# Kernel tuning notes

Measured on AMD Instinct MI355X. Metric: run time of the kernel, lower is better.

## Reference

```python
import jax, jax.numpy as jnp
import numpy as np

B, T, E, H = 8, 2048, 1024, 128

def setup_inputs() -> dict:
    key = jax.random.key(0)
    k1, k2, k3, k4 = jax.random.split(key, 4)
    s = 0.02
    return {
        "x":  jax.random.normal(k1, (B, T, E), dtype=jnp.float32),
        "Wq": jax.random.normal(k2, (E, H), dtype=jnp.float32) * s,
        "Wk": jax.random.normal(k3, (E, H), dtype=jnp.float32) * s,
        "Wv": jax.random.normal(k4, (E, H), dtype=jnp.float32) * s,
    }

def reference(x, Wq, Wk, Wv):
    # q,k,v: [B,T,H]
    q = jnp.einsum("bte,eh->bth", x, Wq)
    k = jnp.einsum("bte,eh->bth", x, Wk)
    v = jnp.einsum("bte,eh->bth", x, Wv)
    scale = jnp.asarray(q.shape[-1], q.dtype) ** -0.5
    wei = jnp.einsum("bqh,bkh->bqk", q, k) * scale  # [B,T,T]
    causal = jnp.tril(jnp.ones((wei.shape[1], wei.shape[2]), dtype=bool))
    wei = jnp.where(causal, wei, jnp.asarray(-jnp.inf, wei.dtype))
    wei = jax.nn.softmax(wei, axis=-1)
    # dropout_prob = 0.0 -> identity
    return jnp.einsum("bqk,bkh->bqh", wei, v)
```

## Files before the change

kernel.cpp:

```cpp
#include <hip/hip_runtime.h>

#define BB 8
#define TT 2048
#define EE 1024
#define HH 128

typedef __bf16 bf16;
typedef __attribute__((ext_vector_type(8))) __bf16 bf16x8;
typedef __attribute__((ext_vector_type(4))) __bf16 bf16x4;
typedef __attribute__((ext_vector_type(4))) float f32x4;
typedef __attribute__((ext_vector_type(16))) float f32x16;

__device__ __host__ inline int qb_off(int qb) {
  int h = qb >> 1;
  return qb + h * (h - 1) + ((qb & 1) ? h : 0);
}
#define NSLAB 72

__device__ inline void gload_lds16(const bf16* g, bf16* l) {
  __builtin_amdgcn_global_load_lds((const __attribute__((address_space(1))) unsigned int*)g,
                                   (__attribute__((address_space(3))) unsigned int*)l,
                                   16, 0, 0);
}

__global__ __launch_bounds__(256) void wt_kernel(const float* __restrict__ wq,
                                                 const float* __restrict__ wk,
                                                 const float* __restrict__ wv,
                                                 bf16* __restrict__ wt) {
  __shared__ float tile[64][65];
  const int z = blockIdx.z;
  const float* w = (z == 0) ? wq : ((z == 1) ? wk : wv);
  const int k0 = blockIdx.x * 64;
  const int h0 = blockIdx.y * 64;
  const int c = threadIdx.x & 63;
  const int r0 = threadIdx.x >> 6;
#pragma unroll
  for (int i = 0; i < 16; ++i) {
    int tt = r0 + i * 4;
    tile[tt][c] = w[(size_t)(k0 + tt) * HH + h0 + c];
  }
  __syncthreads();
#pragma unroll
  for (int i = 0; i < 16; ++i) {
    int hh = r0 + i * 4;
    wt[((size_t)(z * HH + h0 + hh)) * EE + k0 + c] = (bf16)tile[c][hh];
  }
}

__global__ __launch_bounds__(256) void xcvt_kernel(const float* __restrict__ x,
                                                   bf16* __restrict__ xb) {
  const size_t base = (size_t)blockIdx.x * 4096 + threadIdx.x * 4;
#pragma unroll
  for (int j = 0; j < 4; ++j) {
    size_t idx = base + j * 1024;
    f32x4 xv = *(const f32x4*)(x + idx);
    bf16x4 xo;
#pragma unroll
    for (int i = 0; i < 4; ++i) xo[i] = (bf16)xv[i];
    *(bf16x4*)(xb + idx) = xo;
  }
}

__global__ __launch_bounds__(256) void gemm_kernel(const bf16* __restrict__ xb,
                                                   const bf16* __restrict__ wt,
                                                   bf16* __restrict__ q,
                                                   bf16* __restrict__ k,
                                                   bf16* __restrict__ v) {
  __shared__ bf16 As[128 * 32];
  __shared__ bf16 Bs[96 * 32];
  const int tid = threadIdx.x;
  const int lane = tid & 63;
  const int wave = tid >> 6;
  const int l16 = lane & 15;
  const int quad = lane >> 4;
  const int wm = wave & 1;
  const int wn = wave >> 1;
  const int bm = blockIdx.x;
  const int ntile = blockIdx.y;

  const int trow = tid >> 2;
  const int tsub = (tid & 3) * 8;
  const bf16* gA = xb + (size_t)(bm * 128 + trow) * EE + tsub;
  const bf16* gB = wt + (size_t)(ntile * 96 + trow) * EE + tsub;

  f32x4 acc[4][3];
#pragma unroll
  for (int rg = 0; rg < 4; ++rg)
#pragma unroll
    for (int nt = 0; nt < 3; ++nt) acc[rg][nt] = f32x4{0.f, 0.f, 0.f, 0.f};

  for (int ks = 0; ks < EE / 32; ++ks) {
    gload_lds16(gA + ks * 32, &As[wave * 512]);
    gload_lds16(gA + (size_t)64 * EE + ks * 32, &As[2048 + wave * 512]);
    gload_lds16(gB + ks * 32, &Bs[wave * 512]);
    if (tid < 128)
      gload_lds16(gB + (size_t)64 * EE + ks * 32, &Bs[2048 + wave * 512]);
    __syncthreads();

    bf16x8 af[4], bf[3];
#pragma unroll
    for (int rg = 0; rg < 4; ++rg)
      af[rg] = *(const bf16x8*)&As[(wm * 64 + rg * 16 + l16) * 32 + quad * 8];
#pragma unroll
    for (int nt = 0; nt < 3; ++nt)
      bf[nt] = *(const bf16x8*)&Bs[(wn * 48 + nt * 16 + l16) * 32 + quad * 8];
#pragma unroll
    for (int rg = 0; rg < 4; ++rg)
#pragma unroll
      for (int nt = 0; nt < 3; ++nt)
        acc[rg][nt] = __builtin_amdgcn_mfma_f32_16x16x32_bf16(af[rg], bf[nt], acc[rg][nt], 0, 0, 0);
    __syncthreads();
  }

  bf16* outp[3] = {q, k, v};
#pragma unroll
  for (int rg = 0; rg < 4; ++rg)
#pragma unroll
    for (int nt = 0; nt < 3; ++nt) {
      int col = ntile * 96 + wn * 48 + nt * 16 + l16;
      int z = col >> 7;
      int n = col & 127;
#pragma unroll
      for (int r = 0; r < 4; ++r) {
        int row = bm * 128 + wm * 64 + rg * 16 + quad * 4 + r;
        outp[z][(size_t)row * HH + n] = (bf16)acc[rg][nt][r];
      }
    }
}

__global__ __launch_bounds__(256) void vtrans_kernel(const bf16* __restrict__ v,
                                                     bf16* __restrict__ vt) {
  __shared__ bf16 tile[64][65];
  const int b = blockIdx.x;
  const int t0 = blockIdx.y * 64;
  const int h0 = blockIdx.z * 64;
  const int c = threadIdx.x & 63;
  const int r0 = threadIdx.x >> 6;
#pragma unroll
  for (int i = 0; i < 16; ++i) {
    int tt = r0 + i * 4;
    tile[tt][c] = v[((size_t)(b * TT + t0 + tt)) * HH + h0 + c];
  }
  __syncthreads();
#pragma unroll
  for (int i = 0; i < 16; ++i) {
    int hh = r0 + i * 4;
    vt[((size_t)(b * HH + h0 + hh)) * TT + t0 + c] = tile[c][hh];
  }
}


__device__ __forceinline__ unsigned pk2(float a, float b) {
  union { __bf16 h[2]; unsigned u; } x;
  x.h[0] = (__bf16)a;
  x.h[1] = (__bf16)b;
  return x.u;
}

__device__ __forceinline__ void plswap(unsigned& a, unsigned& b) {
  asm volatile("v_permlane32_swap_b32 %0, %1" : "+v"(a), "+v"(b));
}

__global__ __launch_bounds__(256, 2) void flash_kernel(const bf16* __restrict__ q,
                                                       const bf16* __restrict__ k,
                                                       const bf16* __restrict__ vt,
                                                       bf16* __restrict__ opart,
                                                       float* __restrict__ lpart) {
  __shared__ bf16 Ks[64 * 128];
  __shared__ bf16 Vs[128 * 64];

  const int b = blockIdx.x & 7;
  int j = (NSLAB - 1) - (blockIdx.x >> 3);
  int qb = 0, ns = 1;
  while (j >= ns) { j -= ns; ++qb; ns = ((2 * qb + 1) >> 2) + 1; }
  const int s = j;
  const int kt0 = s * 4;
  const int kt1 = min(kt0 + 3, 2 * qb + 1);

  const int tid = threadIdx.x;
  const int lane = tid & 63;
  const int wave = tid >> 6;
  const int l32 = lane & 31;
  const int hi = lane >> 5;
  const int qrow = qb * 128 + wave * 32 + l32;
  const int kdiag = qb * 4 + wave;

  bf16x8 qf[8];
  {
    const bf16* qp = q + (size_t)(b * TT + qrow) * HH + hi * 8;
#pragma unroll
    for (int h16 = 0; h16 < 8; ++h16) qf[h16] = *(const bf16x8*)(qp + h16 * 16);
  }

  f32x16 O[4];
#pragma unroll
  for (int ht = 0; ht < 4; ++ht)
#pragma unroll
    for (int r = 0; r < 16; ++r) O[ht][r] = 0.f;
  float L = 0.f;

  const int krow_s = tid >> 4;
  const int kchk_s = (tid & 15) ^ (krow_s & 7);
  const int vrow_s = tid >> 3;
  const int vchk_s = (tid & 7) ^ (vrow_s & 7);
  const bf16* kg = k + (size_t)b * TT * HH;
  const bf16* vg = vt + (size_t)b * HH * TT;

  const int kxor = (l32 & 7) << 3;
  const float c_ = 0.12753257680406733f;

  for (int kt = kt0; kt <= kt1; ++kt) {
#pragma unroll
    for (int i = 0; i < 4; ++i)
      gload_lds16(kg + (size_t)(kt * 64 + i * 16 + krow_s) * HH + kchk_s * 8,
                  &Ks[(i * 256 + wave * 64) * 8]);
#pragma unroll
    for (int i = 0; i < 4; ++i)
      gload_lds16(vg + (size_t)(i * 32 + vrow_s) * TT + kt * 64 + vchk_s * 8,
                  &Vs[(i * 256 + wave * 64) * 8]);
    __syncthreads();

#pragma unroll
    for (int khalf = 0; khalf < 2; ++khalf) {
      const int k32 = kt * 2 + khalf;
      if (k32 <= kdiag) {
        const bf16* kls = &Ks[(khalf * 32 + l32) * 128];
        bf16x8 kf[8];
#pragma unroll
        for (int h16 = 0; h16 < 8; ++h16)
          kf[h16] = *(const bf16x8*)&kls[(h16 * 16 + hi * 8) ^ kxor];

        f32x16 S;
#pragma unroll
        for (int r = 0; r < 16; ++r) S[r] = 0.f;
        __builtin_amdgcn_s_setprio(1);
#pragma unroll
        for (int h16 = 0; h16 < 8; ++h16)
          S = __builtin_amdgcn_mfma_f32_32x32x16_bf16(kf[h16], qf[h16], S, 0, 0, 0);
        __builtin_amdgcn_s_setprio(0);

        float p[16];
        if (k32 == kdiag) {
          const int kkb = k32 * 32 + 4 * hi;
#pragma unroll
          for (int r = 0; r < 16; ++r) {
            int kk = kkb + (r & 3) + 8 * (r >> 2);
            float pv = (kk <= qrow) ? exp2f(S[r] * c_) : 0.f;
            p[r] = pv;
            L += pv;
          }
        } else {
#pragma unroll
          for (int r = 0; r < 16; ++r) {
            float pv = exp2f(S[r] * c_);
            p[r] = pv;
            L += pv;
          }
        }

#pragma unroll
        for (int s16 = 0; s16 < 2; ++s16) {
          unsigned w0 = pk2(p[s16 * 8 + 0], p[s16 * 8 + 1]);
          unsigned w1 = pk2(p[s16 * 8 + 2], p[s16 * 8 + 3]);
          unsigned w2 = pk2(p[s16 * 8 + 4], p[s16 * 8 + 5]);
          unsigned w3 = pk2(p[s16 * 8 + 6], p[s16 * 8 + 7]);
          plswap(w0, w2);
          plswap(w1, w3);
          union { unsigned u[4]; bf16x8 v; } af;
          af.u[0] = w0;
          af.u[1] = w1;
          af.u[2] = w2;
          af.u[3] = w3;
          bf16x8 vf[4];
#pragma unroll
          for (int ht = 0; ht < 4; ++ht)
            vf[ht] = *(const bf16x8*)&Vs[(l32 + 32 * ht) * 64 +
                                         ((khalf * 32 + s16 * 16 + hi * 8) ^ kxor)];
          __builtin_amdgcn_s_setprio(1);
#pragma unroll
          for (int ht = 0; ht < 4; ++ht)
            O[ht] = __builtin_amdgcn_mfma_f32_32x32x16_bf16(af.v, vf[ht], O[ht], 0, 0, 0);
          __builtin_amdgcn_s_setprio(0);
        }
      }
    }
    __syncthreads();
  }

  L += __shfl_xor(L, 32, 64);

  const size_t slab = (size_t)(b * NSLAB + qb_off(qb) + s);
  bf16* op = opart + slab * (128 * 128) + (size_t)wave * 32 * 128;
#pragma unroll
  for (int ht = 0; ht < 4; ++ht)
#pragma unroll
    for (int r = 0; r < 16; ++r) {
      int qr = (r & 3) + 8 * (r >> 2) + 4 * hi;
      op[qr * 128 + ht * 32 + l32] = (bf16)O[ht][r];
    }
  if (hi == 0) lpart[slab * 128 + wave * 32 + l32] = L;
}

__global__ __launch_bounds__(128) void combine_kernel(const bf16* __restrict__ opart,
                                                      const float* __restrict__ lpart,
                                                      float* __restrict__ out) {
  const int b = blockIdx.x;
  const int qt16 = blockIdx.y;
  const int half = blockIdx.z;
  const int row = threadIdx.x >> 3;
  const int colo = (threadIdx.x & 7) * 8 + half * 64;
  const int qb = qt16 >> 3;
  const int srow = (qt16 & 7) * 16 + row;
  const int ns = ((2 * qb + 1) >> 2) + 1;
  const size_t slab0 = (size_t)(b * NSLAB + qb_off(qb));

  float acc[8];
#pragma unroll
  for (int j = 0; j < 8; ++j) acc[j] = 0.f;
  float L = 0.f;

  int s = 0;
  for (; s + 4 <= ns; s += 4) {
    float l0 = lpart[(slab0 + s + 0) * 128 + srow];
    float l1 = lpart[(slab0 + s + 1) * 128 + srow];
    float l2 = lpart[(slab0 + s + 2) * 128 + srow];
    float l3 = lpart[(slab0 + s + 3) * 128 + srow];
    bf16x8 v0 = *(const bf16x8*)(opart + (slab0 + s + 0) * (128 * 128) + srow * 128 + colo);
    bf16x8 v1 = *(const bf16x8*)(opart + (slab0 + s + 1) * (128 * 128) + srow * 128 + colo);
    bf16x8 v2 = *(const bf16x8*)(opart + (slab0 + s + 2) * (128 * 128) + srow * 128 + colo);
    bf16x8 v3 = *(const bf16x8*)(opart + (slab0 + s + 3) * (128 * 128) + srow * 128 + colo);
    L += (l0 + l1) + (l2 + l3);
#pragma unroll
    for (int j = 0; j < 8; ++j)
      acc[j] += ((float)v0[j] + (float)v1[j]) + ((float)v2[j] + (float)v3[j]);
  }
  for (; s < ns; ++s) {
    L += lpart[(slab0 + s) * 128 + srow];
    bf16x8 ov = *(const bf16x8*)(opart + (slab0 + s) * (128 * 128) + srow * 128 + colo);
#pragma unroll
    for (int j = 0; j < 8; ++j) acc[j] += (float)ov[j];
  }
  float invL = 1.f / L;
  float* o = out + ((size_t)(b * TT + qt16 * 16 + row)) * HH + colo;
  f32x4 o0, o1;
#pragma unroll
  for (int j = 0; j < 4; ++j) { o0[j] = acc[j] * invL; o1[j] = acc[j + 4] * invL; }
  *(f32x4*)o = o0;
  *(f32x4*)(o + 4) = o1;
}

extern "C" void kernel_launch(void* const* d_in, const int* in_sizes, int n_in,
                              void* d_out, int out_size, void* d_ws, size_t ws_size,
                              hipStream_t stream) {
  const float* x = (const float*)d_in[0];
  const float* wq = (const float*)d_in[1];
  const float* wk = (const float*)d_in[2];
  const float* wv = (const float*)d_in[3];
  float* out = (float*)d_out;

  char* ws = (char*)d_ws;
  const size_t NE = (size_t)BB * TT * HH;
  bf16* wt = (bf16*)ws;
  bf16* xb = (bf16*)(ws + (1 << 20));
  bf16* q = (bf16*)(ws + (33 << 20));
  bf16* k = q + NE;
  bf16* v = k + NE;
  bf16* vt = v + NE;
  bf16* opart = xb;
  float* lpart = (float*)(opart + (size_t)(BB * NSLAB) * 128 * 128);

  wt_kernel<<<dim3(16, 2, 3), 256, 0, stream>>>(wq, wk, wv, wt);
  xcvt_kernel<<<dim3(4096), 256, 0, stream>>>(x, xb);
  gemm_kernel<<<dim3(128, 4), 256, 0, stream>>>(xb, wt, q, k, v);
  vtrans_kernel<<<dim3(8, 32, 2), 256, 0, stream>>>(v, vt);
  flash_kernel<<<dim3(576), 256, 0, stream>>>(q, k, vt, opart, lpart);
  combine_kernel<<<dim3(8, 128, 2), 128, 0, stream>>>(opart, lpart, out);
}
```

Before: 158.0 us.

## Double-buffer GEMM and flash LDS tiles, merge weight transpose and x conversion kernels

Adds two-stage LDS double buffering to both the projection GEMM and the flash attention kernel, so the global-to-LDS load for the next tile is issued before computing on the current one, and one barrier per iteration is removed. Also merges the weight-transpose and x-conversion kernels into a single launch to save launch overhead. The flash kernel's LDS use doubles to 64 KB per block, which may limit the two-blocks-per-CU occupancy, and relying on the trailing barrier alone for async LDS loads risks ordering issues.

```diff
diff --git a/kernel.cpp b/kernel.cpp
--- a/kernel.cpp
+++ b/kernel.cpp
@@ -23,41 +23,44 @@
                                    16, 0, 0);
 }
 
-__global__ __launch_bounds__(256) void wt_kernel(const float* __restrict__ wq,
-                                                 const float* __restrict__ wk,
-                                                 const float* __restrict__ wv,
-                                                 bf16* __restrict__ wt) {
+__global__ __launch_bounds__(256) void prep_kernel(const float* __restrict__ x,
+                                                   bf16* __restrict__ xb,
+                                                   const float* __restrict__ wq,
+                                                   const float* __restrict__ wk,
+                                                   const float* __restrict__ wv,
+                                                   bf16* __restrict__ wt) {
   __shared__ float tile[64][65];
-  const int z = blockIdx.z;
-  const float* w = (z == 0) ? wq : ((z == 1) ? wk : wv);
-  const int k0 = blockIdx.x * 64;
-  const int h0 = blockIdx.y * 64;
-  const int c = threadIdx.x & 63;
-  const int r0 = threadIdx.x >> 6;
-#pragma unroll
-  for (int i = 0; i < 16; ++i) {
-    int tt = r0 + i * 4;
-    tile[tt][c] = w[(size_t)(k0 + tt) * HH + h0 + c];
-  }
-  __syncthreads();
-#pragma unroll
-  for (int i = 0; i < 16; ++i) {
-    int hh = r0 + i * 4;
-    wt[((size_t)(z * HH + h0 + hh)) * EE + k0 + c] = (bf16)tile[c][hh];
-  }
-}
-
-__global__ __launch_bounds__(256) void xcvt_kernel(const float* __restrict__ x,
-                                                   bf16* __restrict__ xb) {
-  const size_t base = (size_t)blockIdx.x * 4096 + threadIdx.x * 4;
-#pragma unroll
-  for (int j = 0; j < 4; ++j) {
-    size_t idx = base + j * 1024;
-    f32x4 xv = *(const f32x4*)(x + idx);
-    bf16x4 xo;
-#pragma unroll
-    for (int i = 0; i < 4; ++i) xo[i] = (bf16)xv[i];
-    *(bf16x4*)(xb + idx) = xo;
+  const int bid = blockIdx.x;
+  if (bid < 4096) {
+    const size_t base = (size_t)bid * 4096 + threadIdx.x * 4;
+#pragma unroll
+    for (int j = 0; j < 4; ++j) {
+      size_t idx = base + j * 1024;
+      f32x4 xv = *(const f32x4*)(x + idx);
+      bf16x4 xo;
+#pragma unroll
+      for (int i = 0; i < 4; ++i) xo[i] = (bf16)xv[i];
+      *(bf16x4*)(xb + idx) = xo;
+    }
+  } else {
+    const int id = bid - 4096;
+    const int z = id >> 5;
+    const int h0 = ((id >> 4) & 1) * 64;
+    const int k0 = (id & 15) * 64;
+    const float* w = (z == 0) ? wq : ((z == 1) ? wk : wv);
+    const int c = threadIdx.x & 63;
+    const int r0 = threadIdx.x >> 6;
+#pragma unroll
+    for (int i = 0; i < 16; ++i) {
+      int tt = r0 + i * 4;
+      tile[tt][c] = w[(size_t)(k0 + tt) * HH + h0 + c];
+    }
+    __syncthreads();
+#pragma unroll
+    for (int i = 0; i < 16; ++i) {
+      int hh = r0 + i * 4;
+      wt[((size_t)(z * HH + h0 + hh)) * EE + k0 + c] = (bf16)tile[c][hh];
+    }
   }
 }
 
@@ -66,8 +69,8 @@
                                                    bf16* __restrict__ q,
                                                    bf16* __restrict__ k,
                                                    bf16* __restrict__ v) {
-  __shared__ bf16 As[128 * 32];
-  __shared__ bf16 Bs[96 * 32];
+  __shared__ bf16 As[2][128 * 32];
+  __shared__ bf16 Bs[2][96 * 32];
   const int tid = threadIdx.x;
   const int lane = tid & 63;
   const int wave = tid >> 6;
@@ -89,27 +92,36 @@
 #pragma unroll
     for (int nt = 0; nt < 3; ++nt) acc[rg][nt] = f32x4{0.f, 0.f, 0.f, 0.f};
 
+  auto stage = [&](int bufi, int ks) {
+    gload_lds16(gA + ks * 32, &As[bufi][wave * 512]);
+    gload_lds16(gA + (size_t)64 * EE + ks * 32, &As[bufi][2048 + wave * 512]);
+    gload_lds16(gB + ks * 32, &Bs[bufi][wave * 512]);
+    if (tid < 128)
+      gload_lds16(gB + (size_t)64 * EE + ks * 32, &Bs[bufi][2048 + wave * 512]);
+  };
+
+  stage(0, 0);
+  __syncthreads();
+
+  int buf = 0;
   for (int ks = 0; ks < EE / 32; ++ks) {
-    gload_lds16(gA + ks * 32, &As[wave * 512]);
-    gload_lds16(gA + (size_t)64 * EE + ks * 32, &As[2048 + wave * 512]);
-    gload_lds16(gB + ks * 32, &Bs[wave * 512]);
-    if (tid < 128)
-      gload_lds16(gB + (size_t)64 * EE + ks * 32, &Bs[2048 + wave * 512]);
+    if (ks < EE / 32 - 1) stage(buf ^ 1, ks + 1);
+
+    bf16x8 af[4], bf_[3];
+#pragma unroll
+    for (int rg = 0; rg < 4; ++rg)
+      af[rg] = *(const bf16x8*)&As[buf][(wm * 64 + rg * 16 + l16) * 32 + quad * 8];
+#pragma unroll
+    for (int nt = 0; nt < 3; ++nt)
+      bf_[nt] = *(const bf16x8*)&Bs[buf][(wn * 48 + nt * 16 + l16) * 32 + quad * 8];
+#pragma unroll
+    for (int rg = 0; rg < 4; ++rg)
+#pragma unroll
+      for (int nt = 0; nt < 3; ++nt)
+        acc[rg][nt] = __builtin_amdgcn_mfma_f32_16x16x32_bf16(af[rg], bf_[nt], acc[rg][nt], 0, 0, 0);
+
     __syncthreads();
-
-    bf16x8 af[4], bf[3];
-#pragma unroll
-    for (int rg = 0; rg < 4; ++rg)
-      af[rg] = *(const bf16x8*)&As[(wm * 64 + rg * 16 + l16) * 32 + quad * 8];
-#pragma unroll
-    for (int nt = 0; nt < 3; ++nt)
-      bf[nt] = *(const bf16x8*)&Bs[(wn * 48 + nt * 16 + l16) * 32 + quad * 8];
-#pragma unroll
-    for (int rg = 0; rg < 4; ++rg)
-#pragma unroll
-      for (int nt = 0; nt < 3; ++nt)
-        acc[rg][nt] = __builtin_amdgcn_mfma_f32_16x16x32_bf16(af[rg], bf[nt], acc[rg][nt], 0, 0, 0);
-    __syncthreads();
+    buf ^= 1;
   }
 
   bf16* outp[3] = {q, k, v};
@@ -149,7 +161,6 @@
   }
 }
 
-
 __device__ __forceinline__ unsigned pk2(float a, float b) {
   union { __bf16 h[2]; unsigned u; } x;
   x.h[0] = (__bf16)a;
@@ -166,8 +177,8 @@
                                                        const bf16* __restrict__ vt,
                                                        bf16* __restrict__ opart,
                                                        float* __restrict__ lpart) {
-  __shared__ bf16 Ks[64 * 128];
-  __shared__ bf16 Vs[128 * 64];
+  __shared__ bf16 Ks[2][64 * 128];
+  __shared__ bf16 Vs[2][128 * 64];
 
   const int b = blockIdx.x & 7;
   int j = (NSLAB - 1) - (blockIdx.x >> 3);
@@ -206,25 +217,32 @@
   const bf16* kg = k + (size_t)b * TT * HH;
   const bf16* vg = vt + (size_t)b * HH * TT;
 
+  auto stageKV = [&](int bufi, int kt) {
+#pragma unroll
+    for (int i = 0; i < 4; ++i)
+      gload_lds16(kg + (size_t)(kt * 64 + i * 16 + krow_s) * HH + kchk_s * 8,
+                  &Ks[bufi][(i * 256 + wave * 64) * 8]);
+#pragma unroll
+    for (int i = 0; i < 4; ++i)
+      gload_lds16(vg + (size_t)(i * 32 + vrow_s) * TT + kt * 64 + vchk_s * 8,
+                  &Vs[bufi][(i * 256 + wave * 64) * 8]);
+  };
+
   const int kxor = (l32 & 7) << 3;
   const float c_ = 0.12753257680406733f;
 
+  stageKV(0, kt0);
+  __syncthreads();
+
+  int buf = 0;
   for (int kt = kt0; kt <= kt1; ++kt) {
-#pragma unroll
-    for (int i = 0; i < 4; ++i)
-      gload_lds16(kg + (size_t)(kt * 64 + i * 16 + krow_s) * HH + kchk_s * 8,
-                  &Ks[(i * 256 + wave * 64) * 8]);
-#pragma unroll
-    for (int i = 0; i < 4; ++i)
-      gload_lds16(vg + (size_t)(i * 32 + vrow_s) * TT + kt * 64 + vchk_s * 8,
-                  &Vs[(i * 256 + wave * 64) * 8]);
-    __syncthreads();
+    if (kt < kt1) stageKV(buf ^ 1, kt + 1);
 
 #pragma unroll
     for (int khalf = 0; khalf < 2; ++khalf) {
       const int k32 = kt * 2 + khalf;
       if (k32 <= kdiag) {
-        const bf16* kls = &Ks[(khalf * 32 + l32) * 128];
+        const bf16* kls = &Ks[buf][(khalf * 32 + l32) * 128];
         bf16x8 kf[8];
 #pragma unroll
         for (int h16 = 0; h16 < 8; ++h16)
@@ -274,8 +292,8 @@
           bf16x8 vf[4];
 #pragma unroll
           for (int ht = 0; ht < 4; ++ht)
-            vf[ht] = *(const bf16x8*)&Vs[(l32 + 32 * ht) * 64 +
-                                         ((khalf * 32 + s16 * 16 + hi * 8) ^ kxor)];
+            vf[ht] = *(const bf16x8*)&Vs[buf][(l32 + 32 * ht) * 64 +
+                                             ((khalf * 32 + s16 * 16 + hi * 8) ^ kxor)];
           __builtin_amdgcn_s_setprio(1);
 #pragma unroll
           for (int ht = 0; ht < 4; ++ht)
@@ -285,6 +303,7 @@
       }
     }
     __syncthreads();
+    buf ^= 1;
   }
 
   L += __shfl_xor(L, 32, 64);
@@ -369,8 +388,7 @@
   bf16* opart = xb;
   float* lpart = (float*)(opart + (size_t)(BB * NSLAB) * 128 * 128);
 
-  wt_kernel<<<dim3(16, 2, 3), 256, 0, stream>>>(wq, wk, wv, wt);
-  xcvt_kernel<<<dim3(4096), 256, 0, stream>>>(x, xb);
+  prep_kernel<<<dim3(4192), 256, 0, stream>>>(x, xb, wq, wk, wv, wt);
   gemm_kernel<<<dim3(128, 4), 256, 0, stream>>>(xb, wt, q, k, v);
   vtrans_kernel<<<dim3(8, 32, 2), 256, 0, stream>>>(v, vt);
   flash_kernel<<<dim3(576), 256, 0, stream>>>(q, k, vt, opart, lpart);
```

After: 154.7 us. -2.1%, faster.
